# Kernel tuning notes

Hardware: AMD Instinct MI355X
Metric: run time of the kernel (lower is better)

Reference implementation:

```python
import jax, jax.numpy as jnp
import numpy as np

EPS = 1e-5
CIN = [3, 24, 48, 96, 192]
COUT = [24, 48, 96, 192, 384]
P = 512
NUM_CLASSES = 101
FC_IN = 384 * 16 * 3 * 3  # 55296


def _poly_layer(x, proj, alpha, gamma, beta):
    # x: (B, C, D, H, W)
    B, C, D, H, W = x.shape
    # im2col: 3x3x3 patches with zero padding 1 -> (B, C*27, D, H, W)
    patches = jax.lax.conv_general_dilated_patches(
        x, filter_shape=(3, 3, 3), window_strides=(1, 1, 1),
        padding=[(1, 1), (1, 1), (1, 1)])
    patches = jnp.moveaxis(patches, 1, -1)  # (B, D, H, W, C*27)
    ws = jnp.einsum('bdhwk,pk->bdhwp', patches, proj)      # projector GEMM
    out = jnp.einsum('bdhwp,po->bdhwo', ws, alpha)         # alpha GEMM
    out = jnp.maximum(1.0 + out, 0.0)                      # clamp(1+x, min=0)
    out = jnp.moveaxis(out, -1, 1)                         # (B, O, D, H, W)
    # MaxPool3d kernel/stride (1,2,2)
    out = jax.lax.reduce_window(out, -jnp.inf, jax.lax.max,
                                (1, 1, 1, 2, 2), (1, 1, 1, 2, 2), 'VALID')
    # BatchNorm3d with batch statistics (train-mode math)
    mean = out.mean(axis=(0, 2, 3, 4), keepdims=True)
    var = out.var(axis=(0, 2, 3, 4), keepdims=True)
    out = (out - mean) * jax.lax.rsqrt(var + EPS)
    out = out * gamma.reshape(1, -1, 1, 1, 1) + beta.reshape(1, -1, 1, 1, 1)
    return out


def setup_inputs() -> dict:
    key = jax.random.key(0)
    keys = jax.random.split(key, 32)
    inp = {'x': jax.random.normal(keys[0], (2, 3, 16, 112, 112), dtype=jnp.float32)}
    ki = 1
    for i in range(5):
        k_feat = CIN[i] * 27
        inp[f'p{i+1}'] = jax.random.normal(keys[ki], (P, k_feat), dtype=jnp.float32) / np.sqrt(k_feat); ki += 1
        inp[f'a{i+1}'] = jax.random.normal(keys[ki], (P, COUT[i]), dtype=jnp.float32) * np.sqrt(2.0 / COUT[i]); ki += 1
        inp[f'g{i+1}'] = jnp.ones((COUT[i],), dtype=jnp.float32)
        inp[f'q{i+1}'] = jnp.zeros((COUT[i],), dtype=jnp.float32)
    inp['w1'] = jax.random.normal(keys[ki], (512, FC_IN), dtype=jnp.float32) * np.sqrt(2.0 / 512); ki += 1
    inp['b1'] = jnp.zeros((512,), dtype=jnp.float32)
    inp['w2'] = jax.random.normal(keys[ki], (256, 512), dtype=jnp.float32) * np.sqrt(2.0 / 256); ki += 1
    inp['b2'] = jnp.zeros((256,), dtype=jnp.float32)
    inp['w3'] = jax.random.normal(keys[ki], (NUM_CLASSES, 256), dtype=jnp.float32) * np.sqrt(2.0 / NUM_CLASSES); ki += 1
    inp['b3'] = jnp.zeros((NUM_CLASSES,), dtype=jnp.float32)
    return inp


def reference(x, p1, a1, g1, q1, p2, a2, g2, q2, p3, a3, g3, q3,
              p4, a4, g4, q4, p5, a5, g5, q5, w1, b1, w2, b2, w3, b3):
    projs = [p1, p2, p3, p4, p5]
    alphas = [a1, a2, a3, a4, a5]
    gammas = [g1, g2, g3, g4, g5]
    betas = [q1, q2, q3, q4, q5]
    h = x
    for i in range(5):
        h = _poly_layer(h, projs[i], alphas[i], gammas[i], betas[i])
    h = h.reshape(h.shape[0], -1)  # (B, 55296)
    h = jax.nn.relu(h @ w1.T + b1)  # dropout = identity (eval)
    h = jax.nn.relu(h @ w2.T + b2)
    logits = h @ w3.T + b3
    return logits
```

## Files before the change

kernel.cpp:

```cpp
#include <hip/hip_runtime.h>

#define EPS_BN 1e-5f

typedef __attribute__((ext_vector_type(8))) short sh8;
typedef __attribute__((ext_vector_type(4))) short sh4;
typedef __attribute__((ext_vector_type(4))) float f32x4;

static const size_t WF_OFF[5] = {0, 1944, 33048, 157464, 655128};
static const size_t PART_OFF = 2645784;
static const size_t PRE_OFF  = 6258456;
static const size_t OUT5_OFF = 8666904;
static const size_t H_OFF    = 8777496;
static const size_t ST_OFF   = 8888088;
static const size_t BNP_OFF  = 8888856;
static const size_t H1_OFF   = 8938008;
static const size_t WS_TOT   = 8939032;
__device__ __align__(256) float g_ws[WS_TOT];

static const size_t XIN_OFF = 0;
static const size_t A1_OFF  = 1871424;
static const size_t A2_OFF  = 4776768;
static const size_t A3_OFF  = 6331968;
static const size_t A4_OFF  = 7216704;
static const size_t AR_TOT  = 7776576;
__device__ __align__(256) unsigned short g_act[AR_TOT];

static const size_t WB_OFF[5] = {0, 4096, 36352, 162304, 659968};
__device__ __align__(256) unsigned short g_wb[2650624];

__device__ inline unsigned short f2bf(float v) {
    unsigned u = __float_as_uint(v);
    return (unsigned short)((u + 0x7fffu + ((u >> 16) & 1u)) >> 16);
}

__global__ __launch_bounds__(256) void zero16(int4* __restrict__ p, int n) {
    const int i = blockIdx.x * 256 + threadIdx.x;
    if (i < n) p[i] = make_int4(0, 0, 0, 0);
}

__global__ __launch_bounds__(256) void convert_input(const float* __restrict__ x,
                                                     unsigned short* __restrict__ xp,
                                                     float* __restrict__ bnp)
{
    const int i = blockIdx.x * 256 + threadIdx.x;
    if (i < 49152) bnp[i] = 0.f;
    if (i >= 2 * 18 * 114 * 114 * 4) return;
    const int c = i & 3;
    int t = i >> 2;
    const int xx = t % 114; t /= 114;
    const int yy = t % 114; t /= 114;
    const int zz = t % 18;
    const int b  = t / 18;
    float v = 0.f;
    if (c < 3 && (unsigned)(zz - 1) < 16u && (unsigned)(yy - 1) < 112u && (unsigned)(xx - 1) < 112u)
        v = x[(((size_t)b * 3 + c) * 16 + (zz - 1)) * 12544 + (yy - 1) * 112 + (xx - 1)];
    xp[i] = f2bf(v);
}

struct FuseArgs {
    const float* proj[5];
    const float* alpha[5];
    float* Wf[5];
    int K[5];
    int CO[5];
    int NT[5];
    int start[6];
};

__global__ __launch_bounds__(256) void fuse_all(FuseArgs a)
{
    __shared__ __align__(16) float sa[16][64];
    __shared__ __align__(16) float sp[16][64];

    int l = 0;
    {
        const int bx = blockIdx.x;
        while (l < 4 && bx >= a.start[l + 1]) ++l;
    }
    const int idx = blockIdx.x - a.start[l];
    const int NT = a.NT[l];
    const int obase = (idx / NT) * 64;
    const int kbase = (idx % NT) * 64;
    const int K = a.K[l], CO = a.CO[l];
    const float* __restrict__ proj  = a.proj[l];
    const float* __restrict__ alpha = a.alpha[l];
    float* __restrict__ Wf = a.Wf[l];

    const int tid = threadIdx.x;
    const int tk = tid & 15, to = tid >> 4;

    const int pp  = tid >> 4;
    const int col = (tid & 15) * 4;
    const int o_st = obase + col;
    const int k_st = kbase + col;
    const bool a_ok  = (o_st < CO);
    const bool p_vec = ((K & 3) == 0) && (k_st + 4 <= K);

    float acc[4][4];
    #pragma unroll
    for (int i = 0; i < 4; ++i)
        #pragma unroll
        for (int j = 0; j < 4; ++j) acc[i][j] = 0.f;

    for (int p0 = 0; p0 < 512; p0 += 16) {
        const float* ap  = alpha + (size_t)(p0 + pp) * CO;
        const float* prp = proj  + (size_t)(p0 + pp) * K;
        float4 va = make_float4(0.f, 0.f, 0.f, 0.f);
        float4 vp = make_float4(0.f, 0.f, 0.f, 0.f);
        if (a_ok) va = *(const float4*)(ap + o_st);
        if (p_vec) {
            vp = *(const float4*)(prp + k_st);
        } else {
            float t4[4];
            #pragma unroll
            for (int j = 0; j < 4; ++j)
                t4[j] = (k_st + j < K) ? prp[k_st + j] : 0.f;
            vp = make_float4(t4[0], t4[1], t4[2], t4[3]);
        }
        *(float4*)&sa[pp][col] = va;
        *(float4*)&sp[pp][col] = vp;
        __syncthreads();
        #pragma unroll
        for (int p = 0; p < 16; ++p) {
            const float4 a4 = *(const float4*)&sa[p][to * 4];
            const float4 b4 = *(const float4*)&sp[p][tk * 4];
            const float aa[4] = {a4.x, a4.y, a4.z, a4.w};
            const float bb[4] = {b4.x, b4.y, b4.z, b4.w};
            #pragma unroll
            for (int i = 0; i < 4; ++i)
                #pragma unroll
                for (int j = 0; j < 4; ++j)
                    acc[i][j] = fmaf(aa[i], bb[j], acc[i][j]);
        }
        __syncthreads();
    }

    #pragma unroll
    for (int i = 0; i < 4; ++i) {
        const int o = obase + to * 4 + i;
        if (o < CO) {
            #pragma unroll
            for (int j = 0; j < 4; ++j) {
                const int kk = kbase + tk * 4 + j;
                if (kk < K) Wf[(size_t)o * K + kk] = acc[i][j];
            }
        }
    }
}

struct ReordArgs {
    const float* Wf[5];
    unsigned short* Wb[5];
    int K[5], CPAD[5], KPAD[5], CO[5];
    int start[6];
};

__global__ __launch_bounds__(256) void reorder_all(ReordArgs a)
{
    int l = 0;
    {
        const int bx = blockIdx.x;
        while (l < 4 && bx >= a.start[l + 1]) ++l;
    }
    const int o = blockIdx.x - a.start[l];
    const int K = a.K[l], CPAD = a.CPAD[l], KPAD = a.KPAD[l], CO = a.CO[l];
    const int tid = threadIdx.x;
    unsigned short* row = a.Wb[l] + (size_t)o * KPAD;
    for (int i = tid; i < KPAD; i += 256) row[i] = 0;
    __syncthreads();
    if (o < CO) {
        const float* wr = a.Wf[l] + (size_t)o * K;
        for (int k = tid; k < K; k += 256) {
            const int c = k / 27, s = k - c * 27;
            row[s * CPAD + c] = f2bf(wr[k]);
        }
    }
}

template<int CPAD, int COUT, int KPAD, int HI, int WI, int HP, int WP, int NBLK, int SPLIT>
__global__ __launch_bounds__(256) void conv_mfma(
    const unsigned short* __restrict__ in, const unsigned short* __restrict__ Wb,
    float* __restrict__ outf, float* __restrict__ part, float* __restrict__ bnp)
{
    constexpr int NT = NBLK / 16;
    constexpr int HI2 = HI + 2, WI2 = WI + 2;
    constexpr bool C8 = (CPAD % 8 == 0);
    constexpr int TABN = C8 ? KPAD / 8 : KPAD / 4;
    constexpr int NSTEP = KPAD / 32 / SPLIT;
    constexpr int MTOT = 2 * 16 * HP * WP * 4;

    __shared__ __align__(16) unsigned short As[64 * 40];
    __shared__ __align__(16) unsigned short Bs[NBLK * 40];
    __shared__ int tab[TABN];
    __shared__ float bs[(SPLIT == 1) ? 2 * NBLK : 1];

    const int tid = threadIdx.x;
    const int lane = tid & 63;
    const int wv = tid >> 6;
    const int blk_m = blockIdx.x;
    const int oc0 = blockIdx.y * NBLK;
    const int kc = (SPLIT > 1) ? blockIdx.z : 0;

    for (int i = tid; i < TABN; i += 256) {
        const int k = i * (C8 ? 8 : 4);
        const int s = k / CPAD, c = k % CPAD;
        tab[i] = (s < 27) ? ((((s / 9) * HI2 + (s % 9) / 3) * WI2 + (s % 3)) * CPAD + c) : -1;
    }

    const int m_l = tid & 63;
    const int oct = tid >> 6;
    const int m_g = blk_m * 64 + m_l;
    const int pooled = m_g >> 2, sub = m_g & 3;
    const int pw_g = pooled % WP;
    const int ph_g = (pooled / WP) % HP;
    const int d_g  = (pooled / (WP * HP)) & 15;
    const int b_g  = pooled / (WP * HP * 16);
    const int h_g = 2 * ph_g + (sub >> 1);
    const int w_g = 2 * pw_g + (sub & 1);
    const size_t base_m = ((((size_t)b_g * 18 + d_g) * HI2 + h_g) * WI2 + w_g) * CPAD;

    f32x4 acc[NT];
    #pragma unroll
    for (int i = 0; i < NT; ++i) acc[i] = (f32x4){0.f, 0.f, 0.f, 0.f};

    const int k_begin = kc * NSTEP * 32;
    __syncthreads();

    for (int s = 0; s < NSTEP; ++s) {
        const int k0 = k_begin + s * 32;
        if constexpr (C8) {
            const int off = tab[(k0 >> 3) + oct];
            sh8 av = (sh8){0, 0, 0, 0, 0, 0, 0, 0};
            if (off >= 0) av = *(const sh8*)(in + base_m + off);
            *(sh8*)&As[m_l * 40 + oct * 8] = av;
        } else {
            #pragma unroll
            for (int hh = 0; hh < 2; ++hh) {
                const int off = tab[(k0 >> 2) + oct * 2 + hh];
                sh4 av = (sh4){0, 0, 0, 0};
                if (off >= 0) av = *(const sh4*)(in + base_m + off);
                *(sh4*)&As[m_l * 40 + oct * 8 + hh * 4] = av;
            }
        }
        for (int i = tid; i < NBLK * 4; i += 256) {
            const int row = i >> 2, cc = i & 3;
            *(sh8*)&Bs[row * 40 + cc * 8] =
                *(const sh8*)&Wb[(size_t)(oc0 + row) * KPAD + k0 + cc * 8];
        }
        __syncthreads();
        const sh8 af = *(const sh8*)&As[(wv * 16 + (lane & 15)) * 40 + (lane >> 4) * 8];
        #pragma unroll
        for (int nt = 0; nt < NT; ++nt) {
            const sh8 bf = *(const sh8*)&Bs[(nt * 16 + (lane & 15)) * 40 + (lane >> 4) * 8];
            acc[nt] = __builtin_amdgcn_mfma_f32_16x16x32_bf16(af, bf, acc[nt], 0, 0, 0);
        }
        __syncthreads();
    }

    const int q = lane >> 4;
    const int nloc = lane & 15;
    if constexpr (SPLIT == 1) {
        for (int i = tid; i < 2 * NBLK; i += 256) bs[i] = 0.f;
        __syncthreads();
        const int pooled_o = blk_m * 16 + wv * 4 + q;
        #pragma unroll
        for (int nt = 0; nt < NT; ++nt) {
            const int oc = oc0 + nt * 16 + nloc;
            float mx = fmaxf(1.f + acc[nt][0], 0.f);
            mx = fmaxf(mx, fmaxf(1.f + acc[nt][1], 0.f));
            mx = fmaxf(mx, fmaxf(1.f + acc[nt][2], 0.f));
            mx = fmaxf(mx, fmaxf(1.f + acc[nt][3], 0.f));
            float s1 = 0.f;
            if (oc < COUT) {
                outf[(size_t)pooled_o * COUT + oc] = mx;
                s1 = mx;
            }
            float s2 = s1 * s1;
            s1 += __shfl_xor(s1, 16);
            s1 += __shfl_xor(s1, 32);
            s2 += __shfl_xor(s2, 16);
            s2 += __shfl_xor(s2, 32);
            if (q == 0) {
                atomicAdd(&bs[nt * 16 + nloc], s1);
                atomicAdd(&bs[NBLK + nt * 16 + nloc], s2);
            }
        }
        __syncthreads();
        float* rowp = bnp + (size_t)(blk_m & 63) * 768;
        for (int i = tid; i < NBLK; i += 256) {
            const int oc = oc0 + i;
            if (oc < COUT) {
                atomicAdd(&rowp[oc], bs[i]);
                atomicAdd(&rowp[384 + oc], bs[NBLK + i]);
            }
        }
    } else {
        #pragma unroll
        for (int nt = 0; nt < NT; ++nt) {
            const int oc = oc0 + nt * 16 + nloc;
            #pragma unroll
            for (int r = 0; r < 4; ++r) {
                const int mm = blk_m * 64 + wv * 16 + q * 4 + r;
                part[((size_t)kc * MTOT + mm) * COUT + oc] = acc[nt][r];
            }
        }
    }
}

template<int COUT, int HP, int WP, int SPLIT>
__global__ __launch_bounds__(256) void pool_epi(const float* __restrict__ part,
                                                float* __restrict__ outf,
                                                float* __restrict__ bnp)
{
    constexpr int PO = 2 * 16 * HP * WP;
    constexpr int M = PO * 4;
    __shared__ float bs[2 * COUT];
    const int tid = threadIdx.x;
    for (int i = tid; i < 2 * COUT; i += 256) bs[i] = 0.f;
    __syncthreads();
    const int idx = blockIdx.x * 256 + tid;
    if (idx < PO * COUT) {
        const int oc = idx % COUT;
        const int p = idx / COUT;
        float v[4] = {0.f, 0.f, 0.f, 0.f};
        for (int s = 0; s < SPLIT; ++s)
            #pragma unroll
            for (int r = 0; r < 4; ++r)
                v[r] += part[((size_t)s * M + p * 4 + r) * COUT + oc];
        float mx = fmaxf(1.f + v[0], 0.f);
        mx = fmaxf(mx, fmaxf(1.f + v[1], 0.f));
        mx = fmaxf(mx, fmaxf(1.f + v[2], 0.f));
        mx = fmaxf(mx, fmaxf(1.f + v[3], 0.f));
        outf[(size_t)p * COUT + oc] = mx;
        atomicAdd(&bs[oc], mx);
        atomicAdd(&bs[COUT + oc], mx * mx);
    }
    __syncthreads();
    float* rowp = bnp + (size_t)(blockIdx.x & 63) * 768;
    for (int i = tid; i < COUT; i += 256) {
        atomicAdd(&rowp[i], bs[i]);
        atomicAdd(&rowp[384 + i], bs[COUT + i]);
    }
}

__global__ __launch_bounds__(64) void bn_reduce(float* __restrict__ bnp,
                                                const float* __restrict__ gamma,
                                                const float* __restrict__ beta,
                                                float* __restrict__ st,
                                                float inv_n)
{
    const int c = blockIdx.x, tid = threadIdx.x;
    float s = bnp[(size_t)tid * 768 + c];
    float q = bnp[(size_t)tid * 768 + 384 + c];
    bnp[(size_t)tid * 768 + c] = 0.f;
    bnp[(size_t)tid * 768 + 384 + c] = 0.f;
    #pragma unroll
    for (int off = 32; off > 0; off >>= 1) {
        s += __shfl_down(s, off);
        q += __shfl_down(q, off);
    }
    if (tid == 0) {
        const float mean = s * inv_n;
        const float var  = q * inv_n - mean * mean;
        const float sc   = gamma[c] * rsqrtf(var + EPS_BN);
        st[2 * c]     = sc;
        st[2 * c + 1] = fmaf(-mean, sc, beta[c]);
    }
}

template<int C, int HP, int WP>
__global__ __launch_bounds__(256) void bn_apply_halo(const float* __restrict__ pre,
                                                     const float* __restrict__ st,
                                                     unsigned short* __restrict__ outh)
{
    constexpr int PO = 2 * 16 * HP * WP;
    const int idx = blockIdx.x * 256 + threadIdx.x;
    if (idx >= PO * C) return;
    const int c = idx % C;
    const int p = idx / C;
    const int pw = p % WP;
    const int ph = (p / WP) % HP;
    const int d  = (p / (WP * HP)) & 15;
    const int b  = p / (WP * HP * 16);
    const float v = fmaf(pre[idx], st[2 * c], st[2 * c + 1]);
    outh[((((size_t)b * 18 + d + 1) * (HP + 2) + ph + 1) * (WP + 2) + pw + 1) * C + c] = f2bf(v);
}

__global__ __launch_bounds__(256) void transpose5(const float* __restrict__ out5,
                                                  const float* __restrict__ st,
                                                  float* __restrict__ h)
{
    const int idx = blockIdx.x * 256 + threadIdx.x;
    if (idx >= 110592) return;
    const int c = idx % 384;
    const int p = idx / 384;
    const int b = p / 144;
    const int sp = p % 144;
    h[(size_t)b * 55296 + c * 144 + sp] = fmaf(out5[idx], st[2 * c], st[2 * c + 1]);
}

__global__ __launch_bounds__(256) void fc1_k(const float* __restrict__ h,
                                             const float* __restrict__ w1,
                                             const float* __restrict__ b1,
                                             float* __restrict__ hout)
{
    __shared__ float r0[256];
    __shared__ float r1[256];
    const int j = blockIdx.x, tid = threadIdx.x;
    const float* wr = w1 + (size_t)j * 55296;
    float a0 = 0.f, a1 = 0.f;
    for (int k = tid * 4; k < 55296; k += 1024) {
        const float4 w = *(const float4*)(wr + k);
        const float4 u = *(const float4*)(h + k);
        const float4 v = *(const float4*)(h + 55296 + k);
        a0 += w.x * u.x + w.y * u.y + w.z * u.z + w.w * u.w;
        a1 += w.x * v.x + w.y * v.y + w.z * v.z + w.w * v.w;
    }
    r0[tid] = a0; r1[tid] = a1;
    __syncthreads();
    for (int off = 128; off > 0; off >>= 1) {
        if (tid < off) { r0[tid] += r0[tid + off]; r1[tid] += r1[tid + off]; }
        __syncthreads();
    }
    if (tid == 0) {
        hout[j]       = fmaxf(r0[0] + b1[j], 0.f);
        hout[512 + j] = fmaxf(r1[0] + b1[j], 0.f);
    }
}

__global__ __launch_bounds__(256) void fc23_k(const float* __restrict__ h1,
                                              const float* __restrict__ w2,
                                              const float* __restrict__ b2,
                                              const float* __restrict__ w3,
                                              const float* __restrict__ b3,
                                              float* __restrict__ out)
{
    __shared__ float h1s[1024];
    __shared__ float h2[512];
    const int tid = threadIdx.x;
    for (int i = tid; i < 1024; i += 256) h1s[i] = h1[i];
    __syncthreads();
    {
        const float* wr = w2 + (size_t)tid * 512;
        #pragma unroll
        for (int b = 0; b < 2; ++b) {
            float a = 0.f;
            const float* hh = h1s + b * 512;
            for (int k = 0; k < 512; ++k) a = fmaf(wr[k], hh[k], a);
            h2[b * 256 + tid] = fmaxf(a + b2[tid], 0.f);
        }
    }
    __syncthreads();
    if (tid < 101) {
        const float* wr = w3 + (size_t)tid * 256;
        #pragma unroll
        for (int b = 0; b < 2; ++b) {
            float a = 0.f;
            const float* hh = h2 + b * 256;
            for (int k = 0; k < 256; ++k) a = fmaf(wr[k], hh[k], a);
            out[b * 101 + tid] = a + b3[tid];
        }
    }
}

extern "C" void kernel_launch(void* const* d_in, const int* in_sizes, int n_in,
                              void* d_out, int out_size, void* d_ws, size_t ws_size,
                              hipStream_t stream)
{
    const float* x  = (const float*)d_in[0];
    const float* p[5], *al[5], *g[5], *q[5];
    for (int i = 0; i < 5; ++i) {
        p[i]  = (const float*)d_in[1 + 4 * i];
        al[i] = (const float*)d_in[2 + 4 * i];
        g[i]  = (const float*)d_in[3 + 4 * i];
        q[i]  = (const float*)d_in[4 + 4 * i];
    }
    const float* w1 = (const float*)d_in[21];
    const float* b1 = (const float*)d_in[22];
    const float* w2 = (const float*)d_in[23];
    const float* b2 = (const float*)d_in[24];
    const float* w3 = (const float*)d_in[25];
    const float* b3 = (const float*)d_in[26];

    float* ws = nullptr;
    hipGetSymbolAddress((void**)&ws, HIP_SYMBOL(g_ws));
    unsigned short* act = nullptr;
    hipGetSymbolAddress((void**)&act, HIP_SYMBOL(g_act));
    unsigned short* wb = nullptr;
    hipGetSymbolAddress((void**)&wb, HIP_SYMBOL(g_wb));

    float* Wf[5];
    for (int i = 0; i < 5; ++i) Wf[i] = ws + WF_OFF[i];
    float* part = ws + PART_OFF;
    float* pre  = ws + PRE_OFF;
    float* out5 = ws + OUT5_OFF;
    float* h    = ws + H_OFF;
    float* st   = ws + ST_OFF;
    float* bnp  = ws + BNP_OFF;
    float* h1   = ws + H1_OFF;

    unsigned short* xin = act + XIN_OFF;
    unsigned short* a1  = act + A1_OFF;
    unsigned short* a2  = act + A2_OFF;
    unsigned short* a3  = act + A3_OFF;
    unsigned short* a4  = act + A4_OFF;

    {
        const int n16 = (int)((AR_TOT - A1_OFF) * 2 / 16);
        zero16<<<(n16 + 255) / 256, 256, 0, stream>>>((int4*)(act + A1_OFF), n16);
    }
    convert_input<<<(2 * 18 * 114 * 114 * 4 + 255) / 256, 256, 0, stream>>>(x, xin, bnp);

    static const int KF[5] = {81, 648, 1296, 2592, 5184};
    static const int CO[5] = {24, 48, 96, 192, 384};
    static const int CP[5] = {4, 24, 48, 96, 192};
    static const int KP[5] = {128, 672, 1312, 2592, 5184};
    static const int NPAD[5] = {32, 48, 96, 192, 384};

    FuseArgs fa;
    int s0 = 0;
    for (int i = 0; i < 5; ++i) {
        fa.proj[i] = p[i]; fa.alpha[i] = al[i]; fa.Wf[i] = Wf[i];
        fa.K[i] = KF[i]; fa.CO[i] = CO[i];
        const int nt = (KF[i] + 63) / 64;
        const int mt = (CO[i] + 63) / 64;
        fa.NT[i] = nt;
        fa.start[i] = s0;
        s0 += nt * mt;
    }
    fa.start[5] = s0;
    fuse_all<<<s0, 256, 0, stream>>>(fa);

    ReordArgs ra;
    int r0 = 0;
    for (int i = 0; i < 5; ++i) {
        ra.Wf[i] = Wf[i]; ra.Wb[i] = wb + WB_OFF[i];
        ra.K[i] = KF[i]; ra.CPAD[i] = CP[i]; ra.KPAD[i] = KP[i]; ra.CO[i] = CO[i];
        ra.start[i] = r0;
        r0 += NPAD[i];
    }
    ra.start[5] = r0;
    reorder_all<<<r0, 256, 0, stream>>>(ra);

    conv_mfma<4, 24, 128, 112, 112, 56, 56, 32, 1>
        <<<dim3(6272, 1), 256, 0, stream>>>(xin, wb + WB_OFF[0], pre, nullptr, bnp);
    bn_reduce<<<24, 64, 0, stream>>>(bnp, g[0], q[0], st, 1.f / 100352.f);
    bn_apply_halo<24, 56, 56><<<9408, 256, 0, stream>>>(pre, st, a1);

    conv_mfma<24, 48, 672, 56, 56, 28, 28, 48, 1>
        <<<dim3(1568, 1), 256, 0, stream>>>(a1, wb + WB_OFF[1], pre, nullptr, bnp);
    bn_reduce<<<48, 64, 0, stream>>>(bnp, g[1], q[1], st, 1.f / 25088.f);
    bn_apply_halo<48, 28, 28><<<4704, 256, 0, stream>>>(pre, st, a2);

    conv_mfma<48, 96, 1312, 28, 28, 14, 14, 48, 1>
        <<<dim3(392, 2), 256, 0, stream>>>(a2, wb + WB_OFF[2], pre, nullptr, bnp);
    bn_reduce<<<96, 64, 0, stream>>>(bnp, g[2], q[2], st, 1.f / 6272.f);
    bn_apply_halo<96, 14, 14><<<2352, 256, 0, stream>>>(pre, st, a3);

    conv_mfma<96, 192, 2592, 14, 14, 7, 7, 64, 3>
        <<<dim3(98, 3, 3), 256, 0, stream>>>(a3, wb + WB_OFF[3], nullptr, part, bnp);
    pool_epi<192, 7, 7, 3><<<1176, 256, 0, stream>>>(part, pre, bnp);
    bn_reduce<<<192, 64, 0, stream>>>(bnp, g[3], q[3], st, 1.f / 1568.f);
    bn_apply_halo<192, 7, 7><<<1176, 256, 0, stream>>>(pre, st, a4);

    conv_mfma<192, 384, 5184, 7, 7, 3, 3, 64, 6>
        <<<dim3(18, 6, 6), 256, 0, stream>>>(a4, wb + WB_OFF[4], nullptr, part, bnp);
    pool_epi<384, 3, 3, 6><<<432, 256, 0, stream>>>(part, out5, bnp);
    bn_reduce<<<384, 64, 0, stream>>>(bnp, g[4], q[4], st, 1.f / 288.f);

    transpose5<<<(110592 + 255) / 256, 256, 0, stream>>>(out5, st, h);
    fc1_k<<<512, 256, 0, stream>>>(h, w1, b1, h1);
    fc23_k<<<1, 256, 0, stream>>>(h1, w2, b2, w3, b3, (float*)d_out);
}
```

Before: 540.1 us.

## Double-buffer conv MFMA tiles with register prefetch and merge init kernels

The conv MFMA main loop now uses double-buffered LDS tiles. The next K-step's A and B fragments are loaded into registers before the current MFMAs run and written to the alternate buffer afterwards, so only one barrier per step remains. When the whole weight slice fits in 16 KB, it is loaded into LDS once up front instead of every step. The zero-fill and input-conversion kernels are merged into one launch. This raises LDS use and register pressure, which may lower occupancy.

```diff
diff --git a/kernel.cpp b/kernel.cpp
--- a/kernel.cpp
+++ b/kernel.cpp
@@ -33,16 +33,13 @@
     return (unsigned short)((u + 0x7fffu + ((u >> 16) & 1u)) >> 16);
 }
 
-__global__ __launch_bounds__(256) void zero16(int4* __restrict__ p, int n) {
+__global__ __launch_bounds__(256) void init_input(const float* __restrict__ x,
+                                                  unsigned short* __restrict__ xp,
+                                                  float* __restrict__ bnp,
+                                                  int4* __restrict__ zp, int nz)
+{
     const int i = blockIdx.x * 256 + threadIdx.x;
-    if (i < n) p[i] = make_int4(0, 0, 0, 0);
-}
-
-__global__ __launch_bounds__(256) void convert_input(const float* __restrict__ x,
-                                                     unsigned short* __restrict__ xp,
-                                                     float* __restrict__ bnp)
-{
-    const int i = blockIdx.x * 256 + threadIdx.x;
+    if (i < nz) zp[i] = make_int4(0, 0, 0, 0);
     if (i < 49152) bnp[i] = 0.f;
     if (i >= 2 * 18 * 114 * 114 * 4) return;
     const int c = i & 3;
@@ -188,9 +185,12 @@
     constexpr int TABN = C8 ? KPAD / 8 : KPAD / 4;
     constexpr int NSTEP = KPAD / 32 / SPLIT;
     constexpr int MTOT = 2 * 16 * HP * WP * 4;
-
-    __shared__ __align__(16) unsigned short As[64 * 40];
-    __shared__ __align__(16) unsigned short Bs[NBLK * 40];
+    constexpr bool BONCE = (NBLK * KPAD * 2 <= 16384);
+    constexpr int BROW = BONCE ? (KPAD + 8) : 40;
+    constexpr int BS_ELEMS = BONCE ? NBLK * BROW : 2 * NBLK * 40;
+
+    __shared__ __align__(16) unsigned short As[2][64 * 40];
+    __shared__ __align__(16) unsigned short Bs[BS_ELEMS];
     __shared__ int tab[TABN];
     __shared__ float bs[(SPLIT == 1) ? 2 * NBLK : 1];
 
@@ -205,6 +205,13 @@
         const int k = i * (C8 ? 8 : 4);
         const int s = k / CPAD, c = k % CPAD;
         tab[i] = (s < 27) ? ((((s / 9) * HI2 + (s % 9) / 3) * WI2 + (s % 3)) * CPAD + c) : -1;
+    }
+
+    if constexpr (BONCE) {
+        for (int i = tid; i < NBLK * KPAD / 8; i += 256) {
+            const int r = i / (KPAD / 8), kk = i - r * (KPAD / 8);
+            *(sh8*)&Bs[r * BROW + kk * 8] = *(const sh8*)&Wb[(size_t)(oc0 + r) * KPAD + kk * 8];
+        }
     }
 
     const int m_l = tid & 63;
@@ -219,42 +226,87 @@
     const int w_g = 2 * pw_g + (sub & 1);
     const size_t base_m = ((((size_t)b_g * 18 + d_g) * HI2 + h_g) * WI2 + w_g) * CPAD;
 
+    const int brow = tid >> 2, bcc = tid & 3;
+    const bool bload = (tid < NBLK * 4);
+
     f32x4 acc[NT];
     #pragma unroll
     for (int i = 0; i < NT; ++i) acc[i] = (f32x4){0.f, 0.f, 0.f, 0.f};
 
     const int k_begin = kc * NSTEP * 32;
-    __syncthreads();
-
+
+    sh8 aA; sh4 a0r, a1r; sh8 brg;
+
+    __syncthreads();
+
+    {
+        const int k0 = k_begin;
+        if constexpr (C8) {
+            const int off = tab[(k0 >> 3) + oct];
+            aA = (sh8){0, 0, 0, 0, 0, 0, 0, 0};
+            if (off >= 0) aA = *(const sh8*)(in + base_m + off);
+            *(sh8*)&As[0][m_l * 40 + oct * 8] = aA;
+        } else {
+            const int o0 = tab[(k0 >> 2) + oct * 2];
+            const int o1 = tab[(k0 >> 2) + oct * 2 + 1];
+            a0r = (sh4){0, 0, 0, 0}; a1r = (sh4){0, 0, 0, 0};
+            if (o0 >= 0) a0r = *(const sh4*)(in + base_m + o0);
+            if (o1 >= 0) a1r = *(const sh4*)(in + base_m + o1);
+            *(sh4*)&As[0][m_l * 40 + oct * 8]     = a0r;
+            *(sh4*)&As[0][m_l * 40 + oct * 8 + 4] = a1r;
+        }
+        if constexpr (!BONCE) {
+            if (bload) {
+                brg = *(const sh8*)&Wb[(size_t)(oc0 + brow) * KPAD + k0 + bcc * 8];
+                *(sh8*)&Bs[0 + brow * 40 + bcc * 8] = brg;
+            }
+        }
+    }
+    __syncthreads();
+
+    int cur = 0;
     for (int s = 0; s < NSTEP; ++s) {
         const int k0 = k_begin + s * 32;
-        if constexpr (C8) {
-            const int off = tab[(k0 >> 3) + oct];
-            sh8 av = (sh8){0, 0, 0, 0, 0, 0, 0, 0};
-            if (off >= 0) av = *(const sh8*)(in + base_m + off);
-            *(sh8*)&As[m_l * 40 + oct * 8] = av;
-        } else {
-            #pragma unroll
-            for (int hh = 0; hh < 2; ++hh) {
-                const int off = tab[(k0 >> 2) + oct * 2 + hh];
-                sh4 av = (sh4){0, 0, 0, 0};
-                if (off >= 0) av = *(const sh4*)(in + base_m + off);
-                *(sh4*)&As[m_l * 40 + oct * 8 + hh * 4] = av;
-            }
-        }
-        for (int i = tid; i < NBLK * 4; i += 256) {
-            const int row = i >> 2, cc = i & 3;
-            *(sh8*)&Bs[row * 40 + cc * 8] =
-                *(const sh8*)&Wb[(size_t)(oc0 + row) * KPAD + k0 + cc * 8];
-        }
-        __syncthreads();
-        const sh8 af = *(const sh8*)&As[(wv * 16 + (lane & 15)) * 40 + (lane >> 4) * 8];
+        if (s + 1 < NSTEP) {
+            const int kn = k0 + 32;
+            if constexpr (C8) {
+                const int off = tab[(kn >> 3) + oct];
+                aA = (sh8){0, 0, 0, 0, 0, 0, 0, 0};
+                if (off >= 0) aA = *(const sh8*)(in + base_m + off);
+            } else {
+                const int o0 = tab[(kn >> 2) + oct * 2];
+                const int o1 = tab[(kn >> 2) + oct * 2 + 1];
+                a0r = (sh4){0, 0, 0, 0}; a1r = (sh4){0, 0, 0, 0};
+                if (o0 >= 0) a0r = *(const sh4*)(in + base_m + o0);
+                if (o1 >= 0) a1r = *(const sh4*)(in + base_m + o1);
+            }
+            if constexpr (!BONCE) {
+                if (bload) brg = *(const sh8*)&Wb[(size_t)(oc0 + brow) * KPAD + kn + bcc * 8];
+            }
+        }
+        const sh8 af = *(const sh8*)&As[cur][(wv * 16 + (lane & 15)) * 40 + (lane >> 4) * 8];
         #pragma unroll
         for (int nt = 0; nt < NT; ++nt) {
-            const sh8 bf = *(const sh8*)&Bs[(nt * 16 + (lane & 15)) * 40 + (lane >> 4) * 8];
+            sh8 bf;
+            if constexpr (BONCE)
+                bf = *(const sh8*)&Bs[(nt * 16 + (lane & 15)) * BROW + k0 + (lane >> 4) * 8];
+            else
+                bf = *(const sh8*)&Bs[cur * NBLK * 40 + (nt * 16 + (lane & 15)) * 40 + (lane >> 4) * 8];
             acc[nt] = __builtin_amdgcn_mfma_f32_16x16x32_bf16(af, bf, acc[nt], 0, 0, 0);
         }
+        if (s + 1 < NSTEP) {
+            if constexpr (C8) {
+                *(sh8*)&As[cur ^ 1][m_l * 40 + oct * 8] = aA;
+            } else {
+                *(sh4*)&As[cur ^ 1][m_l * 40 + oct * 8]     = a0r;
+                *(sh4*)&As[cur ^ 1][m_l * 40 + oct * 8 + 4] = a1r;
+            }
+            if constexpr (!BONCE) {
+                if (bload) *(sh8*)&Bs[(cur ^ 1) * NBLK * 40 + brow * 40 + bcc * 8] = brg;
+            }
+        }
         __syncthreads();
+        cur ^= 1;
     }
 
     const int q = lane >> 4;
@@ -506,10 +558,10 @@
     unsigned short* a4  = act + A4_OFF;
 
     {
-        const int n16 = (int)((AR_TOT - A1_OFF) * 2 / 16);
-        zero16<<<(n16 + 255) / 256, 256, 0, stream>>>((int4*)(act + A1_OFF), n16);
-    }
-    convert_input<<<(2 * 18 * 114 * 114 * 4 + 255) / 256, 256, 0, stream>>>(x, xin, bnp);
+        const int nz = (int)((AR_TOT - A1_OFF) * 2 / 16);
+        init_input<<<(2 * 18 * 114 * 114 * 4 + 255) / 256, 256, 0, stream>>>(
+            x, xin, bnp, (int4*)(act + A1_OFF), nz);
+    }
 
     static const int KF[5] = {81, 648, 1296, 2592, 5184};
     static const int CO[5] = {24, 48, 96, 192, 384};
```

After: 511.5 us. -5.3%, faster.
